# Kernel optimization log

Measured on AMD Instinct MI355X. Metric: run time of the kernel, lower is better.

Reference implementation:

```python
import jax, jax.numpy as jnp
import numpy as np

NUM_HASHES = 3
EMBED_DIM = 256
K = 100000          # vocab-size
RATIO = 10          # hash-ratio
B_TABLE = K // RATIO  # 10000; embedding table has B_TABLE + 1 rows
BATCH, SEQ = 32, 2048


def setup_inputs() -> dict:
    key = jax.random.key(0)
    k1, k2, k3 = jax.random.split(key, 3)
    x = jax.random.randint(k1, (BATCH, SEQ, NUM_HASHES), 0, K, dtype=jnp.int64) \
        if jax.config.jax_enable_x64 else \
        jax.random.randint(k1, (BATCH, SEQ, NUM_HASHES), 0, K).astype(jnp.int32)
    emb_table = jax.random.normal(k2, (B_TABLE + 1, EMBED_DIM), dtype=jnp.float32)
    weight_table = jax.random.normal(k3, (K * NUM_HASHES + NUM_HASHES, 1), dtype=jnp.float32)
    return {"x": x, "emb_table": emb_table, "weight_table": weight_table}


def reference(x, emb_table, weight_table):
    # x: [B, S, H] token hashes in [0, K)
    indices = x // RATIO                                   # [B, S, H] -> rows of emb_table
    hash_offsets = (jnp.arange(NUM_HASHES) * (K + 1)).astype(x.dtype)
    weight_idx = x + hash_offsets                          # per-hash salted weight index
    w = weight_table[weight_idx, 0]                        # [B, S, H] per-sample weights
    e = emb_table[indices]                                 # [B, S, H, D] gathered embeddings
    # EmbeddingBag(mode='sum', per_sample_weights): weighted sum over the hash dim
    out = jnp.einsum('bshd,bsh->bsd', e, w)                # [B, S, D]
    return out
```

## Files before the change

kernel.cpp:

```cpp
#include <hip/hip_runtime.h>


#define NUM_HASHES 3
#define EMBED_DIM 256
#define KVOCAB 100000
#define RATIO 10
#define NROWS (KVOCAB / RATIO + 1)
#define QTAB_BYTES ((size_t)NROWS * EMBED_DIM)
#define SCALES_OFF QTAB_BYTES
#define SCALES_BYTES ((size_t)NROWS * 4)
#define WPREP_OFF ((SCALES_OFF + SCALES_BYTES + 255) & ~(size_t)255)
#define QUANT_BLOCKS ((NROWS + 3) / 4)

typedef float f32x4 __attribute__((ext_vector_type(4)));

__device__ __forceinline__ float sbyte_f(unsigned int p, int j) {
    return (float)((signed char)(p >> (8 * j)));
}

__global__ __launch_bounds__(256) void prologue(
    const float* __restrict__ emb,
    const int*   __restrict__ x,
    const float* __restrict__ wt,
    signed char* __restrict__ qt,
    float*       __restrict__ scales,
    float*       __restrict__ wprep,
    int nrows, int T)
{
    if ((int)blockIdx.x < QUANT_BLOCKS) {
        const int row = blockIdx.x * 4 + (threadIdx.x >> 6);
        if (row >= nrows) return;
        const int lane = threadIdx.x & 63;

        f32x4 v = __builtin_nontemporal_load(
            reinterpret_cast<const f32x4*>(emb + (size_t)row * EMBED_DIM) + lane);
        float m = fmaxf(fmaxf(fabsf(v.x), fabsf(v.y)), fmaxf(fabsf(v.z), fabsf(v.w)));
#pragma unroll
        for (int off = 32; off; off >>= 1)
            m = fmaxf(m, __shfl_xor(m, off, 64));

        const float s  = m * (1.0f / 127.0f);
        const float rs = (m > 0.f) ? (127.0f / m) : 0.f;

        const int qx = (int)rintf(v.x * rs);
        const int qy = (int)rintf(v.y * rs);
        const int qz = (int)rintf(v.z * rs);
        const int qw = (int)rintf(v.w * rs);
        const unsigned int packed = (qx & 0xff) | ((qy & 0xff) << 8) |
                                    ((qz & 0xff) << 16) | ((qw & 0xff) << 24);
        reinterpret_cast<unsigned int*>(qt + (size_t)row * EMBED_DIM)[lane] = packed;
        if (lane == 0) scales[row] = s;
    } else {
        const int t = ((int)blockIdx.x - QUANT_BLOCKS) * 256 + (int)threadIdx.x;
        if (t >= T) return;
        const int xv0 = x[(size_t)t * 3 + 0];
        const int xv1 = x[(size_t)t * 3 + 1];
        const int xv2 = x[(size_t)t * 3 + 2];
        wprep[(size_t)t * 3 + 0] = wt[xv0];
        wprep[(size_t)t * 3 + 1] = wt[xv1 + (KVOCAB + 1)];
        wprep[(size_t)t * 3 + 2] = wt[xv2 + 2 * (KVOCAB + 1)];
    }
}

__global__ __launch_bounds__(256) void hash_emb_main(
    const int*         __restrict__ x,
    const signed char* __restrict__ qt,
    const float*       __restrict__ scales,
    const float*       __restrict__ wprep,
    float*             __restrict__ out,
    int T)
{
    int tb = ((blockIdx.x * 256 + threadIdx.x) >> 6) * 4;
    if (tb >= T) return;
    tb = __builtin_amdgcn_readfirstlane(tb);
    const int lane = threadIdx.x & 63;

    const int*   xp = x     + (size_t)tb * 3;
    const float* wp = wprep + (size_t)tb * 3;

    int   xv[12];
    float w[12];
#pragma unroll
    for (int i = 0; i < 12; ++i) { xv[i] = xp[i]; w[i] = wp[i]; }

    unsigned int p[4][3];
    int idx[4][3];
#pragma unroll
    for (int t = 0; t < 4; ++t)
#pragma unroll
        for (int h = 0; h < NUM_HASHES; ++h) {
            idx[t][h] = (int)((unsigned)xv[t * 3 + h] / RATIO);
            p[t][h] = reinterpret_cast<const unsigned int*>(
                          qt + (size_t)idx[t][h] * EMBED_DIM)[lane];
        }

    float ws[4][3];
#pragma unroll
    for (int t = 0; t < 4; ++t)
#pragma unroll
        for (int h = 0; h < NUM_HASHES; ++h)
            ws[t][h] = w[t * 3 + h] * scales[idx[t][h]];

#pragma unroll
    for (int t = 0; t < 4; ++t) {
        f32x4 acc;
        acc.x = sbyte_f(p[t][0], 0) * ws[t][0] + sbyte_f(p[t][1], 0) * ws[t][1] + sbyte_f(p[t][2], 0) * ws[t][2];
        acc.y = sbyte_f(p[t][0], 1) * ws[t][0] + sbyte_f(p[t][1], 1) * ws[t][1] + sbyte_f(p[t][2], 1) * ws[t][2];
        acc.z = sbyte_f(p[t][0], 2) * ws[t][0] + sbyte_f(p[t][1], 2) * ws[t][1] + sbyte_f(p[t][2], 2) * ws[t][2];
        acc.w = sbyte_f(p[t][0], 3) * ws[t][0] + sbyte_f(p[t][1], 3) * ws[t][1] + sbyte_f(p[t][2], 3) * ws[t][2];
        __builtin_nontemporal_store(acc,
            reinterpret_cast<f32x4*>(out + (size_t)(tb + t) * EMBED_DIM) + lane);
    }
}

__global__ __launch_bounds__(256) void hash_emb_f32(
    const int*   __restrict__ x,
    const float* __restrict__ emb,
    const float* __restrict__ wt,
    float*       __restrict__ out,
    int T)
{
    const int token = blockIdx.x * 4 + (threadIdx.x >> 6);
    if (token >= T) return;
    const int lane = threadIdx.x & 63;

    const int* xp = x + (size_t)token * NUM_HASHES;
    f32x4 acc = {0.f, 0.f, 0.f, 0.f};
#pragma unroll
    for (int h = 0; h < NUM_HASHES; ++h) {
        const int   xv = xp[h];
        const float wv = wt[xv + h * (KVOCAB + 1)];
        const f32x4 e  = reinterpret_cast<const f32x4*>(
                             emb + (size_t)((unsigned)xv / RATIO) * EMBED_DIM)[lane];
        acc.x += e.x * wv; acc.y += e.y * wv; acc.z += e.z * wv; acc.w += e.w * wv;
    }
    __builtin_nontemporal_store(acc,
        reinterpret_cast<f32x4*>(out + (size_t)token * EMBED_DIM) + lane);
}

extern "C" void kernel_launch(void* const* d_in, const int* in_sizes, int n_in,
                              void* d_out, int out_size, void* d_ws, size_t ws_size,
                              hipStream_t stream) {
    const int*   x   = (const int*)d_in[0];
    const float* emb = (const float*)d_in[1];
    const float* wt  = (const float*)d_in[2];
    float*       out = (float*)d_out;

    const int T = in_sizes[0] / NUM_HASHES;
    const size_t wprep_bytes = (size_t)T * 3 * 4;
    const size_t ws_need = WPREP_OFF + wprep_bytes;

    if (ws_size >= ws_need) {
        signed char* qt     = (signed char*)d_ws;
        float*       scales = (float*)((char*)d_ws + SCALES_OFF);
        float*       wprep  = (float*)((char*)d_ws + WPREP_OFF);

        const int prep_blocks = (T + 255) / 256;
        hipLaunchKernelGGL(prologue, dim3(QUANT_BLOCKS + prep_blocks), dim3(256), 0, stream,
                           emb, x, wt, qt, scales, wprep, NROWS, T);

        const int waves  = (T + 3) / 4;
        const int blocks = (waves + 3) / 4;
        hipLaunchKernelGGL(hash_emb_main, dim3(blocks), dim3(256), 0, stream,
                           x, qt, scales, wprep, out, T);
    } else {
        const int blocks = (T + 3) / 4;
        hipLaunchKernelGGL(hash_emb_f32, dim3(blocks), dim3(256), 0, stream,
                           x, emb, wt, out, T);
    }
}
```

Baseline: 26.46 us.

## Slice embedding dimension across blocks so each wave covers eight tokens per load

The gather kernel now splits the 256-wide embedding into 8 column slices of 32 bytes. Consecutive blocks handle different slices of the same 64-token group, and each wave processes 16 tokens, with 8 lanes per token and 8 tokens per step. The aim is to change the memory access pattern and the grid shape, possibly improving L2 locality or memory-level parallelism. The cost is 32-byte gathers per row and 128-byte output segments per token in place of full-row coalescing, plus redundant index, weight and scale loads repeated by each slice.

```diff
diff --git a/kernel.cpp b/kernel.cpp
--- a/kernel.cpp
+++ b/kernel.cpp
@@ -11,6 +11,8 @@
 #define SCALES_BYTES ((size_t)NROWS * 4)
 #define WPREP_OFF ((SCALES_OFF + SCALES_BYTES + 255) & ~(size_t)255)
 #define QUANT_BLOCKS ((NROWS + 3) / 4)
+#define TPW 16
+#define TPB (TPW * 4)
 
 typedef float f32x4 __attribute__((ext_vector_type(4)));
 
@@ -62,7 +64,7 @@
     }
 }
 
-__global__ __launch_bounds__(256) void hash_emb_main(
+__global__ __launch_bounds__(256) void hash_emb_sliced(
     const int*         __restrict__ x,
     const signed char* __restrict__ qt,
     const float*       __restrict__ scales,
@@ -70,46 +72,39 @@
     float*             __restrict__ out,
     int T)
 {
-    int tb = ((blockIdx.x * 256 + threadIdx.x) >> 6) * 4;
-    if (tb >= T) return;
-    tb = __builtin_amdgcn_readfirstlane(tb);
-    const int lane = threadIdx.x & 63;
+    const int lane  = threadIdx.x & 63;
+    const int wid   = threadIdx.x >> 6;
+    const int slice = blockIdx.x & 7;
+    const int tb    = (blockIdx.x >> 3) * TPB + wid * TPW;
+    const int sb    = slice * 32 + (lane & 7) * 4;
+#pragma unroll
+    for (int g = 0; g < 2; ++g) {
+        const int tok = tb + g * 8 + (lane >> 3);
+        if (tok >= T) return;
 
-    const int*   xp = x     + (size_t)tb * 3;
-    const float* wp = wprep + (size_t)tb * 3;
+        const int xv0 = x[(size_t)tok * 3 + 0];
+        const int xv1 = x[(size_t)tok * 3 + 1];
+        const int xv2 = x[(size_t)tok * 3 + 2];
+        const int i0 = (int)((unsigned)xv0 / RATIO);
+        const int i1 = (int)((unsigned)xv1 / RATIO);
+        const int i2 = (int)((unsigned)xv2 / RATIO);
 
-    int   xv[12];
-    float w[12];
-#pragma unroll
-    for (int i = 0; i < 12; ++i) { xv[i] = xp[i]; w[i] = wp[i]; }
+        const unsigned int p0 = *reinterpret_cast<const unsigned int*>(qt + (size_t)i0 * EMBED_DIM + sb);
+        const unsigned int p1 = *reinterpret_cast<const unsigned int*>(qt + (size_t)i1 * EMBED_DIM + sb);
+        const unsigned int p2 = *reinterpret_cast<const unsigned int*>(qt + (size_t)i2 * EMBED_DIM + sb);
 
-    unsigned int p[4][3];
-    int idx[4][3];
-#pragma unroll
-    for (int t = 0; t < 4; ++t)
-#pragma unroll
-        for (int h = 0; h < NUM_HASHES; ++h) {
-            idx[t][h] = (int)((unsigned)xv[t * 3 + h] / RATIO);
-            p[t][h] = reinterpret_cast<const unsigned int*>(
-                          qt + (size_t)idx[t][h] * EMBED_DIM)[lane];
-        }
+        const float ws0 = wprep[(size_t)tok * 3 + 0] * scales[i0];
+        const float ws1 = wprep[(size_t)tok * 3 + 1] * scales[i1];
+        const float ws2 = wprep[(size_t)tok * 3 + 2] * scales[i2];
 
-    float ws[4][3];
-#pragma unroll
-    for (int t = 0; t < 4; ++t)
-#pragma unroll
-        for (int h = 0; h < NUM_HASHES; ++h)
-            ws[t][h] = w[t * 3 + h] * scales[idx[t][h]];
+        f32x4 acc;
+        acc.x = sbyte_f(p0, 0) * ws0 + sbyte_f(p1, 0) * ws1 + sbyte_f(p2, 0) * ws2;
+        acc.y = sbyte_f(p0, 1) * ws0 + sbyte_f(p1, 1) * ws1 + sbyte_f(p2, 1) * ws2;
+        acc.z = sbyte_f(p0, 2) * ws0 + sbyte_f(p1, 2) * ws1 + sbyte_f(p2, 2) * ws2;
+        acc.w = sbyte_f(p0, 3) * ws0 + sbyte_f(p1, 3) * ws1 + sbyte_f(p2, 3) * ws2;
 
-#pragma unroll
-    for (int t = 0; t < 4; ++t) {
-        f32x4 acc;
-        acc.x = sbyte_f(p[t][0], 0) * ws[t][0] + sbyte_f(p[t][1], 0) * ws[t][1] + sbyte_f(p[t][2], 0) * ws[t][2];
-        acc.y = sbyte_f(p[t][0], 1) * ws[t][0] + sbyte_f(p[t][1], 1) * ws[t][1] + sbyte_f(p[t][2], 1) * ws[t][2];
-        acc.z = sbyte_f(p[t][0], 2) * ws[t][0] + sbyte_f(p[t][1], 2) * ws[t][1] + sbyte_f(p[t][2], 2) * ws[t][2];
-        acc.w = sbyte_f(p[t][0], 3) * ws[t][0] + sbyte_f(p[t][1], 3) * ws[t][1] + sbyte_f(p[t][2], 3) * ws[t][2];
         __builtin_nontemporal_store(acc,
-            reinterpret_cast<f32x4*>(out + (size_t)(tb + t) * EMBED_DIM) + lane);
+            reinterpret_cast<f32x4*>(out + (size_t)tok * EMBED_DIM + sb));
     }
 }
 
@@ -159,9 +154,8 @@
         hipLaunchKernelGGL(prologue, dim3(QUANT_BLOCKS + prep_blocks), dim3(256), 0, stream,
                            emb, x, wt, qt, scales, wprep, NROWS, T);
 
-        const int waves  = (T + 3) / 4;
-        const int blocks = (waves + 3) / 4;
-        hipLaunchKernelGGL(hash_emb_main, dim3(blocks), dim3(256), 0, stream,
+        const int blocks = ((T + TPB - 1) / TPB) * 8;
+        hipLaunchKernelGGL(hash_emb_sliced, dim3(blocks), dim3(256), 0, stream,
                            x, qt, scales, wprep, out, T);
     } else {
         const int blocks = (T + 3) / 4;
```

After: 31.18 us. 1.18x slower.

## Stage int8 table column slices in LDS and gather from shared memory

Applied to the files above, without the earlier changes.

Adds a main kernel in which each 1024-thread block copies a 16-byte column slice of every quantized table row into LDS. Rows are rotated by row index to spread bank accesses, and the block then serves a 4096-token chunk's gathers from LDS instead of global memory. The intent is to replace scattered global/L2 gathers with LDS reads. The cost is a large per-block table load, one block per CU because each needs about 160KB of LDS, and output stores that become 64-byte segments per token. A fallback kernel that reads weights straight from the weight table is used if the LDS size attribute cannot be set.

```diff
diff --git a/kernel.cpp b/kernel.cpp
--- a/kernel.cpp
+++ b/kernel.cpp
@@ -11,6 +11,9 @@
 #define SCALES_BYTES ((size_t)NROWS * 4)
 #define WPREP_OFF ((SCALES_OFF + SCALES_BYTES + 255) & ~(size_t)255)
 #define QUANT_BLOCKS ((NROWS + 3) / 4)
+#define NSLICES 16
+#define CHUNK_TOKENS 4096
+#define LDS_BYTES (NROWS * 16)
 
 typedef float f32x4 __attribute__((ext_vector_type(4)));
 
@@ -62,7 +65,7 @@
     }
 }
 
-__global__ __launch_bounds__(256) void hash_emb_main(
+__global__ __launch_bounds__(1024) void hash_emb_lds(
     const int*         __restrict__ x,
     const signed char* __restrict__ qt,
     const float*       __restrict__ scales,
@@ -70,18 +73,83 @@
     float*             __restrict__ out,
     int T)
 {
+    extern __shared__ unsigned char lds_raw[];
+    unsigned int* lds32 = reinterpret_cast<unsigned int*>(lds_raw);
+
+    const int slice = blockIdx.x & (NSLICES - 1);
+    const int chunk = blockIdx.x >> 4;
+
+    for (int r = threadIdx.x; r < NROWS; r += 1024) {
+        const uint4 v = *reinterpret_cast<const uint4*>(
+                            qt + (size_t)r * EMBED_DIM + slice * 16);
+        const int rot = r & 3;
+        uint4 w;
+        if      (rot == 0) w = v;
+        else if (rot == 1) w = make_uint4(v.w, v.x, v.y, v.z);
+        else if (rot == 2) w = make_uint4(v.z, v.w, v.x, v.y);
+        else               w = make_uint4(v.y, v.z, v.w, v.x);
+        reinterpret_cast<uint4*>(lds_raw + (size_t)r * 16)[0] = w;
+    }
+    __syncthreads();
+
+    const int lane = threadIdx.x & 63;
+    const int wid  = threadIdx.x >> 6;
+    const int slot = lane & 3;
+    const int tsub = lane >> 2;
+
+#pragma unroll 2
+    for (int it = 0; it < CHUNK_TOKENS / 256; ++it) {
+        const int tok = chunk * CHUNK_TOKENS + it * 256 + wid * 16 + tsub;
+        if (tok >= T) continue;
+
+        const int xv0 = x[(size_t)tok * 3 + 0];
+        const int xv1 = x[(size_t)tok * 3 + 1];
+        const int xv2 = x[(size_t)tok * 3 + 2];
+        const float w0 = wprep[(size_t)tok * 3 + 0];
+        const float w1 = wprep[(size_t)tok * 3 + 1];
+        const float w2 = wprep[(size_t)tok * 3 + 2];
+
+        const int i0 = (int)((unsigned)xv0 / RATIO);
+        const int i1 = (int)((unsigned)xv1 / RATIO);
+        const int i2 = (int)((unsigned)xv2 / RATIO);
+
+        const unsigned int p0 = lds32[i0 * 4 + ((slot + i0) & 3)];
+        const unsigned int p1 = lds32[i1 * 4 + ((slot + i1) & 3)];
+        const unsigned int p2 = lds32[i2 * 4 + ((slot + i2) & 3)];
+
+        const float ws0 = w0 * scales[i0];
+        const float ws1 = w1 * scales[i1];
+        const float ws2 = w2 * scales[i2];
+
+        f32x4 acc;
+        acc.x = sbyte_f(p0, 0) * ws0 + sbyte_f(p1, 0) * ws1 + sbyte_f(p2, 0) * ws2;
+        acc.y = sbyte_f(p0, 1) * ws0 + sbyte_f(p1, 1) * ws1 + sbyte_f(p2, 1) * ws2;
+        acc.z = sbyte_f(p0, 2) * ws0 + sbyte_f(p1, 2) * ws1 + sbyte_f(p2, 2) * ws2;
+        acc.w = sbyte_f(p0, 3) * ws0 + sbyte_f(p1, 3) * ws1 + sbyte_f(p2, 3) * ws2;
+
+        __builtin_nontemporal_store(acc,
+            reinterpret_cast<f32x4*>(out + (size_t)tok * EMBED_DIM
+                                         + slice * 16 + slot * 4));
+    }
+}
+
+__global__ __launch_bounds__(256) void hash_emb_i8x4(
+    const int*         __restrict__ x,
+    const signed char* __restrict__ qt,
+    const float*       __restrict__ scales,
+    const float*       __restrict__ wt,
+    float*             __restrict__ out,
+    int T)
+{
     int tb = ((blockIdx.x * 256 + threadIdx.x) >> 6) * 4;
     if (tb >= T) return;
     tb = __builtin_amdgcn_readfirstlane(tb);
     const int lane = threadIdx.x & 63;
 
-    const int*   xp = x     + (size_t)tb * 3;
-    const float* wp = wprep + (size_t)tb * 3;
-
-    int   xv[12];
-    float w[12];
-#pragma unroll
-    for (int i = 0; i < 12; ++i) { xv[i] = xp[i]; w[i] = wp[i]; }
+    const int* xp = x + (size_t)tb * NUM_HASHES;
+    int xv[12];
+#pragma unroll
+    for (int i = 0; i < 12; ++i) xv[i] = xp[i];
 
     unsigned int p[4][3];
     int idx[4][3];
@@ -99,7 +167,7 @@
     for (int t = 0; t < 4; ++t)
 #pragma unroll
         for (int h = 0; h < NUM_HASHES; ++h)
-            ws[t][h] = w[t * 3 + h] * scales[idx[t][h]];
+            ws[t][h] = wt[xv[t * 3 + h] + h * (KVOCAB + 1)] * scales[idx[t][h]];
 
 #pragma unroll
     for (int t = 0; t < 4; ++t) {
@@ -159,10 +227,21 @@
         hipLaunchKernelGGL(prologue, dim3(QUANT_BLOCKS + prep_blocks), dim3(256), 0, stream,
                            emb, x, wt, qt, scales, wprep, NROWS, T);
 
-        const int waves  = (T + 3) / 4;
-        const int blocks = (waves + 3) / 4;
-        hipLaunchKernelGGL(hash_emb_main, dim3(blocks), dim3(256), 0, stream,
-                           x, qt, scales, wprep, out, T);
+        const hipError_t attr_err = hipFuncSetAttribute(
+            (const void*)hash_emb_lds,
+            hipFuncAttributeMaxDynamicSharedMemorySize, LDS_BYTES);
+
+        if (attr_err == hipSuccess) {
+            const int chunks = (T + CHUNK_TOKENS - 1) / CHUNK_TOKENS;
+            hipLaunchKernelGGL(hash_emb_lds, dim3(chunks * NSLICES), dim3(1024),
+                               LDS_BYTES, stream,
+                               x, qt, scales, wprep, out, T);
+        } else {
+            const int waves  = (T + 3) / 4;
+            const int blocks = (waves + 3) / 4;
+            hipLaunchKernelGGL(hash_emb_i8x4, dim3(blocks), dim3(256), 0, stream,
+                               x, qt, scales, wt, out, T);
+        }
     } else {
         const int blocks = (T + 3) / 4;
         hipLaunchKernelGGL(hash_emb_f32, dim3(blocks), dim3(256), 0, stream,
```

After: 46.05 us. +74.0%, slower.
